# Kernel optimization log

Hardware: AMD Instinct MI355X
Metric: run time of the kernel (lower is better)

The kernel has to match this reference:

```python
import jax, jax.numpy as jnp
import numpy as np

B, T, C, H = 4096, 64, 128, 64  # batch, seq (== blok_olcusu), embed (yerlesdirme_olcusu), head size


def setup_inputs() -> dict:
    key = jax.random.key(0)
    kx, kq, kk, kv = jax.random.split(key, 4)
    x = jax.random.normal(kx, (B, T, C), dtype=jnp.float32)
    # Linear(C, H, bias=False); stored as [in, out] so projection is x @ W
    Wq = jax.random.normal(kq, (C, H), dtype=jnp.float32) * (C ** -0.5)
    Wk = jax.random.normal(kk, (C, H), dtype=jnp.float32) * (C ** -0.5)
    Wv = jax.random.normal(kv, (C, H), dtype=jnp.float32) * (C ** -0.5)
    return {"x": x, "Wq": Wq, "Wk": Wk, "Wv": Wv}


def reference(x, Wq, Wk, Wv):
    _, t, c = x.shape
    q = jnp.einsum("btc,ch->bth", x, Wq)
    k = jnp.einsum("btc,ch->bth", x, Wk)
    v = jnp.einsum("btc,ch->bth", x, Wv)
    # NOTE: source scales by C**-0.5 where C is the EMBEDDING dim, not head size
    scores = jnp.einsum("bth,bsh->bts", q, k) * (c ** -0.5)  # [B, T, T]
    causal = jnp.tril(jnp.ones((t, t), dtype=bool))
    scores = jnp.where(causal, scores, -jnp.inf)
    attn = jax.nn.softmax(scores, axis=-1)
    # dropout is identity in eval mode
    out = jnp.einsum("bts,bsh->bth", attn, v)  # [B, T, H]
    return out
```

## Files before the change

### kernel.cpp

```cpp
#include <hip/hip_runtime.h>
#include <stdint.h>

#define NB 4096
#define TT 64
#define CC 128
#define HH 64
#define BPB 4

typedef __bf16 bf16x8 __attribute__((ext_vector_type(8)));
typedef float f32x4 __attribute__((ext_vector_type(4)));
typedef unsigned short us4 __attribute__((ext_vector_type(4)));

__device__ __forceinline__ unsigned short f2bf(float f) {
  union { float f; uint32_t u; } a; a.f = f;
  uint32_t u = a.u;
  u += 0x7fffu + ((u >> 16) & 1u);
  return (unsigned short)(u >> 16);
}

__device__ __forceinline__ unsigned short bfbits(float f) {
  union { __bf16 b; unsigned short u; } c; c.b = (__bf16)f; return c.u;
}

__device__ __forceinline__ bf16x8 cv8(f32x4 lo, f32x4 hi) {
  bf16x8 v;
  #pragma unroll
  for (int j = 0; j < 4; ++j) { v[j] = (__bf16)lo[j]; v[j + 4] = (__bf16)hi[j]; }
  return v;
}

__global__ void swizzle_w_kernel(const float* __restrict__ Wq,
                                 const float* __restrict__ Wk,
                                 const float* __restrict__ Wv,
                                 unsigned short* __restrict__ wz) {
  int i = blockIdx.x * 256 + threadIdx.x;
  if (i >= 3 * 16 * 64) return;
  int mat  = i >> 10;
  int rem  = i & 1023;
  int frag = rem >> 6;
  int lane = rem & 63;
  int nt = frag >> 2, ks = frag & 3;
  int quad = lane >> 4, l15 = lane & 15;
  int h  = nt * 16 + l15;
  int c0 = ks * 32 + quad * 8;
  const float* W = (mat == 0) ? Wq : (mat == 1) ? Wk : Wv;
  unsigned short* o = wz + (size_t)i * 8;
  #pragma unroll
  for (int j = 0; j < 8; ++j) o[j] = f2bf(W[(c0 + j) * HH + h]);
}

#define MFMA16(A, B, C) __builtin_amdgcn_mfma_f32_16x16x32_bf16((A), (B), (C), 0, 0, 0)

__global__ __launch_bounds__(256, 2)
void attn_kernel(const float* __restrict__ x,
                 const unsigned short* __restrict__ wz,
                 float* __restrict__ out) {
  __shared__ unsigned short qbuf[2][64 * 64];
  __shared__ unsigned short kbuf[2][64 * 64];
  __shared__ unsigned short vbuf[2][64 * 64];

  const int tid  = threadIdx.x;
  const int wave = tid >> 6;
  const int lane = tid & 63;
  const int quad = lane >> 4;
  const int l15  = lane & 15;
  const int l7   = l15 & 7;
  const int mbase = wave * 16;
  const float scale = 0.08838834764831845f;

  const unsigned short* wb = wz + (size_t)lane * 8;
#define WLOAD(P, K) (*(const bf16x8*)(wb + ((size_t)((wave * 3 + (P)) * 4 + (K)) << 9)))
  bf16x8 w00 = WLOAD(0, 0), w01 = WLOAD(0, 1), w02 = WLOAD(0, 2), w03 = WLOAD(0, 3);
  bf16x8 w10 = WLOAD(1, 0), w11 = WLOAD(1, 1), w12 = WLOAD(1, 2), w13 = WLOAD(1, 3);
  bf16x8 w20 = WLOAD(2, 0), w21 = WLOAD(2, 1), w22 = WLOAD(2, 2), w23 = WLOAD(2, 3);
#undef WLOAD

#define PROJ1(P, MT, QSB, KSB, VTB) do {                                     \
    f32x4 acc_ = {0.f, 0.f, 0.f, 0.f};                                       \
    acc_ = MFMA16(xf0_, w##P##0, acc_);                                      \
    acc_ = MFMA16(xf1_, w##P##1, acc_);                                      \
    acc_ = MFMA16(xf2_, w##P##2, acc_);                                      \
    acc_ = MFMA16(xf3_, w##P##3, acc_);                                      \
    const int pi_ = wave * 3 + (P);                                          \
    const int mat_ = pi_ >> 2, nt_ = pi_ & 3;                                \
    if (mat_ == 2) {                                                         \
                   \
      const int h_  = (nt_ << 4) + l15;                                      \
      const int t0_ = ((MT) << 4) + (quad << 2);                             \
      us4 pk_;                                                               \
      pk_[0] = bfbits(acc_[0]); pk_[1] = bfbits(acc_[1]);                    \
      pk_[2] = bfbits(acc_[2]); pk_[3] = bfbits(acc_[3]);                    \
      *(us4*)&(VTB)[(h_ << 6) + (((t0_ >> 3) ^ (h_ & 7)) << 3) + (t0_ & 7)] = pk_; \
    } else {                                                                 \
      unsigned short* dst_ = (mat_ == 0) ? (QSB) : (KSB);                    \
      const int col_ = (nt_ << 4) + l15;                                     \
      const int ch_ = col_ >> 3, cj_ = col_ & 7;                             \
      _Pragma("unroll")                                                      \
      for (int r_ = 0; r_ < 4; ++r_) {                                       \
        const int row_ = ((MT) << 4) + (quad << 2) + r_;                     \
        (dst_)[(row_ << 6) + ((ch_ ^ (row_ & 7)) << 3) + cj_] = bfbits(acc_[r_]); \
      }                                                                      \
    }                                                                        \
  } while (0)

#define DO_PROJ(BB, QSB, KSB, VTB) do {                                      \
    _Pragma("unroll")                                                        \
    for (int mt_ = 0; mt_ < 4; ++mt_) {                                      \
      const float* xr_ = x + ((size_t)(BB) * TT + mt_ * 16 + l15) * CC + quad * 8; \
      const f32x4 a0_ = *(const f32x4*)(xr_);       const f32x4 b0_ = *(const f32x4*)(xr_ + 4);  \
      const f32x4 a1_ = *(const f32x4*)(xr_ + 32);  const f32x4 b1_ = *(const f32x4*)(xr_ + 36); \
      const f32x4 a2_ = *(const f32x4*)(xr_ + 64);  const f32x4 b2_ = *(const f32x4*)(xr_ + 68); \
      const f32x4 a3_ = *(const f32x4*)(xr_ + 96);  const f32x4 b3_ = *(const f32x4*)(xr_ + 100);\
      const bf16x8 xf0_ = cv8(a0_, b0_), xf1_ = cv8(a1_, b1_);               \
      const bf16x8 xf2_ = cv8(a2_, b2_), xf3_ = cv8(a3_, b3_);               \
      PROJ1(0, mt_, QSB, KSB, VTB);                                          \
      PROJ1(1, mt_, QSB, KSB, VTB);                                          \
      PROJ1(2, mt_, QSB, KSB, VTB);                                          \
    }                                                                        \
  } while (0)

#define QK1(NT, SC, KSB) do {                                                \
    const bf16x8 bk0_ = *(const bf16x8*)&(KSB)[((((NT) << 4) + l15) << 6) + ((quad ^ l7) << 3)]; \
    const bf16x8 bk1_ = *(const bf16x8*)&(KSB)[((((NT) << 4) + l15) << 6) + (((4 + quad) ^ l7) << 3)]; \
    SC = MFMA16(aq0_, bk0_, SC);                                             \
    SC = MFMA16(aq1_, bk1_, SC);                                             \
  } while (0)

#define PV1(NT, QSB, VTB) do {                                               \
    const bf16x8 bv0_ = *(const bf16x8*)&(VTB)[((((NT) << 4) + l15) << 6) + ((quad ^ l7) << 3)]; \
    const bf16x8 bv1_ = *(const bf16x8*)&(VTB)[((((NT) << 4) + l15) << 6) + (((4 + quad) ^ l7) << 3)]; \
    f32x4 acc_ = {0.f, 0.f, 0.f, 0.f};                                       \
    acc_ = MFMA16(ap0_, bv0_, acc_);                                         \
    acc_ = MFMA16(ap1_, bv1_, acc_);                                         \
    _Pragma("unroll")                                                        \
    for (int r_ = 0; r_ < 4; ++r_)                                           \
      ob_[(mbase + (quad << 2) + r_) * HH + ((NT) << 4) + l15] = acc_[r_];   \
  } while (0)

#define DO_ATTN(BB, QSB, KSB, VTB) do {                                      \
    const bf16x8 aq0_ = *(const bf16x8*)&(QSB)[((mbase + l15) << 6) + ((quad ^ l7) << 3)]; \
    const bf16x8 aq1_ = *(const bf16x8*)&(QSB)[((mbase + l15) << 6) + (((4 + quad) ^ l7) << 3)]; \
    f32x4 sc0_ = {0.f, 0.f, 0.f, 0.f}, sc1_ = sc0_, sc2_ = sc0_, sc3_ = sc0_; \
    QK1(0, sc0_, KSB); QK1(1, sc1_, KSB); QK1(2, sc2_, KSB); QK1(3, sc3_, KSB); \
    _Pragma("unroll")                                                        \
    for (int r_ = 0; r_ < 4; ++r_) {                                         \
      const int row_ = mbase + (quad << 2) + r_;                             \
      float v0_ = (l15      <= row_) ? sc0_[r_] * scale : -__builtin_inff(); \
      float v1_ = (l15 + 16 <= row_) ? sc1_[r_] * scale : -__builtin_inff(); \
      float v2_ = (l15 + 32 <= row_) ? sc2_[r_] * scale : -__builtin_inff(); \
      float v3_ = (l15 + 48 <= row_) ? sc3_[r_] * scale : -__builtin_inff(); \
      float m_ = fmaxf(fmaxf(v0_, v1_), fmaxf(v2_, v3_));                    \
      _Pragma("unroll")                                                      \
      for (int d_ = 1; d_ < 16; d_ <<= 1) m_ = fmaxf(m_, __shfl_xor(m_, d_, 64)); \
      v0_ = __expf(v0_ - m_); v1_ = __expf(v1_ - m_);                        \
      v2_ = __expf(v2_ - m_); v3_ = __expf(v3_ - m_);                        \
      float s_ = (v0_ + v1_) + (v2_ + v3_);                                  \
      _Pragma("unroll")                                                      \
      for (int d_ = 1; d_ < 16; d_ <<= 1) s_ += __shfl_xor(s_, d_, 64);      \
      const float inv_ = 1.f / s_;                                           \
      const int rs_ = row_ & 7;                                              \
       \
      (QSB)[(row_ << 6) + ((( (l15 >> 3)    ) ^ rs_) << 3) + (l15 & 7)] = bfbits(v0_ * inv_); \
      (QSB)[(row_ << 6) + ((((l15 >> 3) + 2) ^ rs_) << 3) + (l15 & 7)] = bfbits(v1_ * inv_); \
      (QSB)[(row_ << 6) + ((((l15 >> 3) + 4) ^ rs_) << 3) + (l15 & 7)] = bfbits(v2_ * inv_); \
      (QSB)[(row_ << 6) + ((((l15 >> 3) + 6) ^ rs_) << 3) + (l15 & 7)] = bfbits(v3_ * inv_); \
    }                                                                        \
    const bf16x8 ap0_ = *(const bf16x8*)&(QSB)[((mbase + l15) << 6) + ((quad ^ l7) << 3)]; \
    const bf16x8 ap1_ = *(const bf16x8*)&(QSB)[((mbase + l15) << 6) + (((4 + quad) ^ l7) << 3)]; \
    float* ob_ = out + (size_t)(BB) * TT * HH;                               \
    PV1(0, QSB, VTB); PV1(1, QSB, VTB); PV1(2, QSB, VTB); PV1(3, QSB, VTB);  \
  } while (0)

  const int b0 = blockIdx.x * BPB;

  DO_PROJ(b0, qbuf[0], kbuf[0], vbuf[0]);
  __syncthreads();

  #pragma unroll
  for (int bi = 0; bi < BPB; ++bi) {
    const int cu_ = bi & 1;
    if (bi < BPB - 1) DO_PROJ(b0 + bi + 1, qbuf[cu_ ^ 1], kbuf[cu_ ^ 1], vbuf[cu_ ^ 1]);
    DO_ATTN(b0 + bi, qbuf[cu_], kbuf[cu_], vbuf[cu_]);
    __syncthreads();
  }
}

extern "C" void kernel_launch(void* const* d_in, const int* in_sizes, int n_in,
                              void* d_out, int out_size, void* d_ws, size_t ws_size,
                              hipStream_t stream) {
  const float* x  = (const float*)d_in[0];
  const float* Wq = (const float*)d_in[1];
  const float* Wk = (const float*)d_in[2];
  const float* Wv = (const float*)d_in[3];
  unsigned short* wz = (unsigned short*)d_ws;
  float* outp = (float*)d_out;

  swizzle_w_kernel<<<(3 * 16 * 64 + 255) / 256, 256, 0, stream>>>(Wq, Wk, Wv, wz);
  attn_kernel<<<NB / BPB, 256, 0, stream>>>(x, wz, outp);
}
```

Measured before the change: 251.5 us.

## Process one batch per single-wave block, removing cross-wave sync and double buffering

Replaces the 4-wave, 4-batch-per-block kernel (with double-buffered Q/K/V shared memory and __syncthreads) with a single-wave block per batch element. That wave computes all projections, keeps the x fragments in registers, and reuses two 8KB LDS buffers in sequence: Q, then K, then P and V^T. The aim is to remove barriers, cut LDS per block and raise the number of resident blocks. The cost is more weight loads per batch, since each wave reloads all 48 weight fragments, along with higher register pressure and no overlap between projection and attention within a block.

```diff
diff --git a/kernel.cpp b/kernel.cpp
--- a/kernel.cpp
+++ b/kernel.cpp
@@ -5,7 +5,6 @@
 #define TT 64
 #define CC 128
 #define HH 64
-#define BPB 4
 
 typedef __bf16 bf16x8 __attribute__((ext_vector_type(8)));
 typedef float f32x4 __attribute__((ext_vector_type(4)));
@@ -51,138 +50,142 @@
 
 #define MFMA16(A, B, C) __builtin_amdgcn_mfma_f32_16x16x32_bf16((A), (B), (C), 0, 0, 0)
 
-__global__ __launch_bounds__(256, 2)
+#define LDB(BUF, ROW, CH) (*(const bf16x8*)&(BUF)[((ROW) << 6) + (((CH) ^ ((ROW) & 7)) << 3)])
+
+__global__ __launch_bounds__(64, 2)
 void attn_kernel(const float* __restrict__ x,
                  const unsigned short* __restrict__ wz,
                  float* __restrict__ out) {
-  __shared__ unsigned short qbuf[2][64 * 64];
-  __shared__ unsigned short kbuf[2][64 * 64];
-  __shared__ unsigned short vbuf[2][64 * 64];
-
-  const int tid  = threadIdx.x;
-  const int wave = tid >> 6;
-  const int lane = tid & 63;
+  __shared__ unsigned short bufA[64 * 64];
+  __shared__ unsigned short bufB[64 * 64];
+
+  const int lane = threadIdx.x & 63;
   const int quad = lane >> 4;
   const int l15  = lane & 15;
-  const int l7   = l15 & 7;
-  const int mbase = wave * 16;
   const float scale = 0.08838834764831845f;
-
+  const int b = blockIdx.x;
   const unsigned short* wb = wz + (size_t)lane * 8;
-#define WLOAD(P, K) (*(const bf16x8*)(wb + ((size_t)((wave * 3 + (P)) * 4 + (K)) << 9)))
-  bf16x8 w00 = WLOAD(0, 0), w01 = WLOAD(0, 1), w02 = WLOAD(0, 2), w03 = WLOAD(0, 3);
-  bf16x8 w10 = WLOAD(1, 0), w11 = WLOAD(1, 1), w12 = WLOAD(1, 2), w13 = WLOAD(1, 3);
-  bf16x8 w20 = WLOAD(2, 0), w21 = WLOAD(2, 1), w22 = WLOAD(2, 2), w23 = WLOAD(2, 3);
-#undef WLOAD
-
-#define PROJ1(P, MT, QSB, KSB, VTB) do {                                     \
-    f32x4 acc_ = {0.f, 0.f, 0.f, 0.f};                                       \
-    acc_ = MFMA16(xf0_, w##P##0, acc_);                                      \
-    acc_ = MFMA16(xf1_, w##P##1, acc_);                                      \
-    acc_ = MFMA16(xf2_, w##P##2, acc_);                                      \
-    acc_ = MFMA16(xf3_, w##P##3, acc_);                                      \
-    const int pi_ = wave * 3 + (P);                                          \
-    const int mat_ = pi_ >> 2, nt_ = pi_ & 3;                                \
-    if (mat_ == 2) {                                                         \
-                   \
-      const int h_  = (nt_ << 4) + l15;                                      \
-      const int t0_ = ((MT) << 4) + (quad << 2);                             \
-      us4 pk_;                                                               \
-      pk_[0] = bfbits(acc_[0]); pk_[1] = bfbits(acc_[1]);                    \
-      pk_[2] = bfbits(acc_[2]); pk_[3] = bfbits(acc_[3]);                    \
-      *(us4*)&(VTB)[(h_ << 6) + (((t0_ >> 3) ^ (h_ & 7)) << 3) + (t0_ & 7)] = pk_; \
-    } else {                                                                 \
-      unsigned short* dst_ = (mat_ == 0) ? (QSB) : (KSB);                    \
-      const int col_ = (nt_ << 4) + l15;                                     \
-      const int ch_ = col_ >> 3, cj_ = col_ & 7;                             \
-      _Pragma("unroll")                                                      \
-      for (int r_ = 0; r_ < 4; ++r_) {                                       \
-        const int row_ = ((MT) << 4) + (quad << 2) + r_;                     \
-        (dst_)[(row_ << 6) + ((ch_ ^ (row_ & 7)) << 3) + cj_] = bfbits(acc_[r_]); \
-      }                                                                      \
-    }                                                                        \
+
+#define XFRAG(MT) \
+  bf16x8 xf##MT##0, xf##MT##1, xf##MT##2, xf##MT##3; \
+  { const float* xr_ = x + ((size_t)b * TT + (MT) * 16 + l15) * CC + (quad << 3); \
+    const f32x4 p0_ = *(const f32x4*)(xr_);      const f32x4 q0_ = *(const f32x4*)(xr_ + 4);   \
+    const f32x4 p1_ = *(const f32x4*)(xr_ + 32); const f32x4 q1_ = *(const f32x4*)(xr_ + 36);  \
+    const f32x4 p2_ = *(const f32x4*)(xr_ + 64); const f32x4 q2_ = *(const f32x4*)(xr_ + 68);  \
+    const f32x4 p3_ = *(const f32x4*)(xr_ + 96); const f32x4 q3_ = *(const f32x4*)(xr_ + 100); \
+    xf##MT##0 = cv8(p0_, q0_); xf##MT##1 = cv8(p1_, q1_); \
+    xf##MT##2 = cv8(p2_, q2_); xf##MT##3 = cv8(p3_, q3_); }
+  XFRAG(0) XFRAG(1) XFRAG(2) XFRAG(3)
+#undef XFRAG
+
+#define WL(M, NT, KS) (*(const bf16x8*)(wb + (((size_t)(M) * 16 + (NT) * 4 + (KS)) << 9)))
+
+#define WRROW(BUF, MT, NT, ACC) do { \
+    const int h_ = ((NT) << 4) + l15; \
+    const int ch_ = h_ >> 3, cj_ = h_ & 7; \
+    _Pragma("unroll") \
+    for (int r_ = 0; r_ < 4; ++r_) { \
+      const int t_ = ((MT) << 4) + (quad << 2) + r_; \
+      (BUF)[(t_ << 6) + ((ch_ ^ (t_ & 7)) << 3) + cj_] = bfbits(ACC[r_]); \
+    } } while (0)
+
+#define WRVT(BUF, MT, NT, ACC) do { \
+    const int h_  = ((NT) << 4) + l15; \
+    const int t0_ = ((MT) << 4) + (quad << 2); \
+    us4 pk_; pk_[0] = bfbits(ACC[0]); pk_[1] = bfbits(ACC[1]); \
+    pk_[2] = bfbits(ACC[2]); pk_[3] = bfbits(ACC[3]); \
+    *(us4*)&(BUF)[(h_ << 6) + (((t0_ >> 3) ^ (h_ & 7)) << 3) + (t0_ & 7)] = pk_; \
   } while (0)
 
-#define DO_PROJ(BB, QSB, KSB, VTB) do {                                      \
-    _Pragma("unroll")                                                        \
-    for (int mt_ = 0; mt_ < 4; ++mt_) {                                      \
-      const float* xr_ = x + ((size_t)(BB) * TT + mt_ * 16 + l15) * CC + quad * 8; \
-      const f32x4 a0_ = *(const f32x4*)(xr_);       const f32x4 b0_ = *(const f32x4*)(xr_ + 4);  \
-      const f32x4 a1_ = *(const f32x4*)(xr_ + 32);  const f32x4 b1_ = *(const f32x4*)(xr_ + 36); \
-      const f32x4 a2_ = *(const f32x4*)(xr_ + 64);  const f32x4 b2_ = *(const f32x4*)(xr_ + 68); \
-      const f32x4 a3_ = *(const f32x4*)(xr_ + 96);  const f32x4 b3_ = *(const f32x4*)(xr_ + 100);\
-      const bf16x8 xf0_ = cv8(a0_, b0_), xf1_ = cv8(a1_, b1_);               \
-      const bf16x8 xf2_ = cv8(a2_, b2_), xf3_ = cv8(a3_, b3_);               \
-      PROJ1(0, mt_, QSB, KSB, VTB);                                          \
-      PROJ1(1, mt_, QSB, KSB, VTB);                                          \
-      PROJ1(2, mt_, QSB, KSB, VTB);                                          \
-    }                                                                        \
+#define PTILE(MT, NT, WRM, BUF) { \
+    f32x4 acc_ = {0.f, 0.f, 0.f, 0.f}; \
+    acc_ = MFMA16(xf##MT##0, w##NT##0_, acc_); \
+    acc_ = MFMA16(xf##MT##1, w##NT##1_, acc_); \
+    acc_ = MFMA16(xf##MT##2, w##NT##2_, acc_); \
+    acc_ = MFMA16(xf##MT##3, w##NT##3_, acc_); \
+    WRM(BUF, MT, NT, acc_); }
+
+#define PROJ(M, WRM, BUF) do { \
+    const bf16x8 w00_ = WL(M,0,0), w01_ = WL(M,0,1), w02_ = WL(M,0,2), w03_ = WL(M,0,3); \
+    const bf16x8 w10_ = WL(M,1,0), w11_ = WL(M,1,1), w12_ = WL(M,1,2), w13_ = WL(M,1,3); \
+    const bf16x8 w20_ = WL(M,2,0), w21_ = WL(M,2,1), w22_ = WL(M,2,2), w23_ = WL(M,2,3); \
+    const bf16x8 w30_ = WL(M,3,0), w31_ = WL(M,3,1), w32_ = WL(M,3,2), w33_ = WL(M,3,3); \
+    PTILE(0,0,WRM,BUF) PTILE(0,1,WRM,BUF) PTILE(0,2,WRM,BUF) PTILE(0,3,WRM,BUF) \
+    PTILE(1,0,WRM,BUF) PTILE(1,1,WRM,BUF) PTILE(1,2,WRM,BUF) PTILE(1,3,WRM,BUF) \
+    PTILE(2,0,WRM,BUF) PTILE(2,1,WRM,BUF) PTILE(2,2,WRM,BUF) PTILE(2,3,WRM,BUF) \
+    PTILE(3,0,WRM,BUF) PTILE(3,1,WRM,BUF) PTILE(3,2,WRM,BUF) PTILE(3,3,WRM,BUF) \
   } while (0)
 
-#define QK1(NT, SC, KSB) do {                                                \
-    const bf16x8 bk0_ = *(const bf16x8*)&(KSB)[((((NT) << 4) + l15) << 6) + ((quad ^ l7) << 3)]; \
-    const bf16x8 bk1_ = *(const bf16x8*)&(KSB)[((((NT) << 4) + l15) << 6) + (((4 + quad) ^ l7) << 3)]; \
-    SC = MFMA16(aq0_, bk0_, SC);                                             \
-    SC = MFMA16(aq1_, bk1_, SC);                                             \
-  } while (0)
-
-#define PV1(NT, QSB, VTB) do {                                               \
-    const bf16x8 bv0_ = *(const bf16x8*)&(VTB)[((((NT) << 4) + l15) << 6) + ((quad ^ l7) << 3)]; \
-    const bf16x8 bv1_ = *(const bf16x8*)&(VTB)[((((NT) << 4) + l15) << 6) + (((4 + quad) ^ l7) << 3)]; \
-    f32x4 acc_ = {0.f, 0.f, 0.f, 0.f};                                       \
-    acc_ = MFMA16(ap0_, bv0_, acc_);                                         \
-    acc_ = MFMA16(ap1_, bv1_, acc_);                                         \
-    _Pragma("unroll")                                                        \
-    for (int r_ = 0; r_ < 4; ++r_)                                           \
-      ob_[(mbase + (quad << 2) + r_) * HH + ((NT) << 4) + l15] = acc_[r_];   \
-  } while (0)
-
-#define DO_ATTN(BB, QSB, KSB, VTB) do {                                      \
-    const bf16x8 aq0_ = *(const bf16x8*)&(QSB)[((mbase + l15) << 6) + ((quad ^ l7) << 3)]; \
-    const bf16x8 aq1_ = *(const bf16x8*)&(QSB)[((mbase + l15) << 6) + (((4 + quad) ^ l7) << 3)]; \
-    f32x4 sc0_ = {0.f, 0.f, 0.f, 0.f}, sc1_ = sc0_, sc2_ = sc0_, sc3_ = sc0_; \
-    QK1(0, sc0_, KSB); QK1(1, sc1_, KSB); QK1(2, sc2_, KSB); QK1(3, sc3_, KSB); \
-    _Pragma("unroll")                                                        \
-    for (int r_ = 0; r_ < 4; ++r_) {                                         \
-      const int row_ = mbase + (quad << 2) + r_;                             \
-      float v0_ = (l15      <= row_) ? sc0_[r_] * scale : -__builtin_inff(); \
-      float v1_ = (l15 + 16 <= row_) ? sc1_[r_] * scale : -__builtin_inff(); \
-      float v2_ = (l15 + 32 <= row_) ? sc2_[r_] * scale : -__builtin_inff(); \
-      float v3_ = (l15 + 48 <= row_) ? sc3_[r_] * scale : -__builtin_inff(); \
-      float m_ = fmaxf(fmaxf(v0_, v1_), fmaxf(v2_, v3_));                    \
-      _Pragma("unroll")                                                      \
+  PROJ(0, WRROW, bufA);
+  PROJ(1, WRROW, bufB);
+
+  const bf16x8 kb00 = LDB(bufB,      l15, quad), kb01 = LDB(bufB,      l15, 4 + quad);
+  const bf16x8 kb10 = LDB(bufB, 16 + l15, quad), kb11 = LDB(bufB, 16 + l15, 4 + quad);
+  const bf16x8 kb20 = LDB(bufB, 32 + l15, quad), kb21 = LDB(bufB, 32 + l15, 4 + quad);
+  const bf16x8 kb30 = LDB(bufB, 48 + l15, quad), kb31 = LDB(bufB, 48 + l15, 4 + quad);
+
+#define QKMT(MT) do { \
+    const int tb_ = (MT) << 4; \
+    const bf16x8 qa0_ = LDB(bufA, tb_ + l15, quad); \
+    const bf16x8 qa1_ = LDB(bufA, tb_ + l15, 4 + quad); \
+    f32x4 s0_ = {0.f, 0.f, 0.f, 0.f}, s1_ = s0_, s2_ = s0_, s3_ = s0_; \
+    s0_ = MFMA16(qa0_, kb00, s0_); s0_ = MFMA16(qa1_, kb01, s0_); \
+    s1_ = MFMA16(qa0_, kb10, s1_); s1_ = MFMA16(qa1_, kb11, s1_); \
+    s2_ = MFMA16(qa0_, kb20, s2_); s2_ = MFMA16(qa1_, kb21, s2_); \
+    s3_ = MFMA16(qa0_, kb30, s3_); s3_ = MFMA16(qa1_, kb31, s3_); \
+    _Pragma("unroll") \
+    for (int r_ = 0; r_ < 4; ++r_) { \
+      const int row_ = tb_ + (quad << 2) + r_; \
+      float v0_ = (l15      <= row_) ? s0_[r_] * scale : -__builtin_inff(); \
+      float v1_ = (l15 + 16 <= row_) ? s1_[r_] * scale : -__builtin_inff(); \
+      float v2_ = (l15 + 32 <= row_) ? s2_[r_] * scale : -__builtin_inff(); \
+      float v3_ = (l15 + 48 <= row_) ? s3_[r_] * scale : -__builtin_inff(); \
+      float m_ = fmaxf(fmaxf(v0_, v1_), fmaxf(v2_, v3_)); \
+      _Pragma("unroll") \
       for (int d_ = 1; d_ < 16; d_ <<= 1) m_ = fmaxf(m_, __shfl_xor(m_, d_, 64)); \
-      v0_ = __expf(v0_ - m_); v1_ = __expf(v1_ - m_);                        \
-      v2_ = __expf(v2_ - m_); v3_ = __expf(v3_ - m_);                        \
-      float s_ = (v0_ + v1_) + (v2_ + v3_);                                  \
-      _Pragma("unroll")                                                      \
-      for (int d_ = 1; d_ < 16; d_ <<= 1) s_ += __shfl_xor(s_, d_, 64);      \
-      const float inv_ = 1.f / s_;                                           \
-      const int rs_ = row_ & 7;                                              \
-       \
-      (QSB)[(row_ << 6) + ((( (l15 >> 3)    ) ^ rs_) << 3) + (l15 & 7)] = bfbits(v0_ * inv_); \
-      (QSB)[(row_ << 6) + ((((l15 >> 3) + 2) ^ rs_) << 3) + (l15 & 7)] = bfbits(v1_ * inv_); \
-      (QSB)[(row_ << 6) + ((((l15 >> 3) + 4) ^ rs_) << 3) + (l15 & 7)] = bfbits(v2_ * inv_); \
-      (QSB)[(row_ << 6) + ((((l15 >> 3) + 6) ^ rs_) << 3) + (l15 & 7)] = bfbits(v3_ * inv_); \
-    }                                                                        \
-    const bf16x8 ap0_ = *(const bf16x8*)&(QSB)[((mbase + l15) << 6) + ((quad ^ l7) << 3)]; \
-    const bf16x8 ap1_ = *(const bf16x8*)&(QSB)[((mbase + l15) << 6) + (((4 + quad) ^ l7) << 3)]; \
-    float* ob_ = out + (size_t)(BB) * TT * HH;                               \
-    PV1(0, QSB, VTB); PV1(1, QSB, VTB); PV1(2, QSB, VTB); PV1(3, QSB, VTB);  \
-  } while (0)
-
-  const int b0 = blockIdx.x * BPB;
-
-  DO_PROJ(b0, qbuf[0], kbuf[0], vbuf[0]);
-  __syncthreads();
-
-  #pragma unroll
-  for (int bi = 0; bi < BPB; ++bi) {
-    const int cu_ = bi & 1;
-    if (bi < BPB - 1) DO_PROJ(b0 + bi + 1, qbuf[cu_ ^ 1], kbuf[cu_ ^ 1], vbuf[cu_ ^ 1]);
-    DO_ATTN(b0 + bi, qbuf[cu_], kbuf[cu_], vbuf[cu_]);
-    __syncthreads();
-  }
+      v0_ = __expf(v0_ - m_); v1_ = __expf(v1_ - m_); \
+      v2_ = __expf(v2_ - m_); v3_ = __expf(v3_ - m_); \
+      float sm_ = (v0_ + v1_) + (v2_ + v3_); \
+      _Pragma("unroll") \
+      for (int d_ = 1; d_ < 16; d_ <<= 1) sm_ += __shfl_xor(sm_, d_, 64); \
+      const float inv_ = 1.f / sm_; \
+      const int rs_ = row_ & 7; \
+      const int base_ = (row_ << 6) + (l15 & 7); \
+      const int lh_ = l15 >> 3; \
+      bufA[base_ + (((lh_    ) ^ rs_) << 3)] = bfbits(v0_ * inv_); \
+      bufA[base_ + (((lh_ + 2) ^ rs_) << 3)] = bfbits(v1_ * inv_); \
+      bufA[base_ + (((lh_ + 4) ^ rs_) << 3)] = bfbits(v2_ * inv_); \
+      bufA[base_ + (((lh_ + 6) ^ rs_) << 3)] = bfbits(v3_ * inv_); \
+    } } while (0)
+
+  QKMT(0); QKMT(1); QKMT(2); QKMT(3);
+
+  PROJ(2, WRVT, bufB);
+
+  const bf16x8 vb00 = LDB(bufB,      l15, quad), vb01 = LDB(bufB,      l15, 4 + quad);
+  const bf16x8 vb10 = LDB(bufB, 16 + l15, quad), vb11 = LDB(bufB, 16 + l15, 4 + quad);
+  const bf16x8 vb20 = LDB(bufB, 32 + l15, quad), vb21 = LDB(bufB, 32 + l15, 4 + quad);
+  const bf16x8 vb30 = LDB(bufB, 48 + l15, quad), vb31 = LDB(bufB, 48 + l15, 4 + quad);
+
+#define PVMT(MT) do { \
+    const int tb_ = (MT) << 4; \
+    const bf16x8 pa0_ = LDB(bufA, tb_ + l15, quad); \
+    const bf16x8 pa1_ = LDB(bufA, tb_ + l15, 4 + quad); \
+    f32x4 o0_ = {0.f, 0.f, 0.f, 0.f}, o1_ = o0_, o2_ = o0_, o3_ = o0_; \
+    o0_ = MFMA16(pa0_, vb00, o0_); o0_ = MFMA16(pa1_, vb01, o0_); \
+    o1_ = MFMA16(pa0_, vb10, o1_); o1_ = MFMA16(pa1_, vb11, o1_); \
+    o2_ = MFMA16(pa0_, vb20, o2_); o2_ = MFMA16(pa1_, vb21, o2_); \
+    o3_ = MFMA16(pa0_, vb30, o3_); o3_ = MFMA16(pa1_, vb31, o3_); \
+    float* ob_ = out + ((size_t)b * TT + tb_ + (quad << 2)) * HH + l15; \
+    _Pragma("unroll") \
+    for (int r_ = 0; r_ < 4; ++r_) { \
+      ob_[r_ * HH     ] = o0_[r_]; \
+      ob_[r_ * HH + 16] = o1_[r_]; \
+      ob_[r_ * HH + 32] = o2_[r_]; \
+      ob_[r_ * HH + 48] = o3_[r_]; \
+    } } while (0)
+
+  PVMT(0); PVMT(1); PVMT(2); PVMT(3);
 }
 
 extern "C" void kernel_launch(void* const* d_in, const int* in_sizes, int n_in,
@@ -196,5 +199,5 @@
   float* outp = (float*)d_out;
 
   swizzle_w_kernel<<<(3 * 16 * 64 + 255) / 256, 256, 0, stream>>>(Wq, Wk, Wv, wz);
-  attn_kernel<<<NB / BPB, 256, 0, stream>>>(x, wz, outp);
-}
+  attn_kernel<<<NB, 64, 0, stream>>>(x, wz, outp);
+}
```

New measurement: 236.0 us. 6.2% less time.
